# Kernel optimization log

Measured on AMD Instinct MI355X. Metric: run time of the kernel, lower is better.

The kernel has to match this reference:

```python
import jax, jax.numpy as jnp
import numpy as np

CHUNK = 2048  # query chunk for KNN to avoid materializing full NxN distance matrix


def _knn_single(pos, k):
    # pos: [N,3] -> idx [N,k] of k nearest neighbors (incl. self)
    N = pos.shape[0]
    qs = pos.reshape(N // CHUNK, CHUNK, 3)

    def per_chunk(q):
        d = jnp.sum((q[:, None, :] - pos[None, :, :]) ** 2, axis=-1)  # [CHUNK,N]
        _, idx = jax.lax.top_k(-d, k)
        return idx

    return jax.lax.map(per_chunk, qs).reshape(N, k)


def setup_inputs() -> dict:
    key = jax.random.key(0)
    ks = jax.random.split(key, 8)
    B, N, Cin, Cout, H, K = 2, 16384, 32, 64, 128, 16
    Ein = 2 * Cin + 3  # in_feat + out(self)_feat + rel_pos

    def lin(k_, fi, fo):
        return jax.random.normal(k_, (fi, fo), jnp.float32) / np.sqrt(fi)

    return dict(
        positions=jax.random.uniform(ks[0], (B, N, 3), jnp.float32),
        features=jax.random.normal(ks[1], (B, N, Cin), jnp.float32),
        W1=lin(ks[2], Ein, H), b1=jnp.zeros((H,), jnp.float32),
        W2=lin(ks[3], H, Cout), b2=jnp.zeros((Cout,), jnp.float32),
        W3=lin(ks[4], Cout, H), b3=jnp.zeros((H,), jnp.float32),
        W4=lin(ks[5], H, Cout), b4=jnp.zeros((Cout,), jnp.float32),
        knn_k=K,
    )


def reference(positions, features, W1, b1, W2, b2, W3, b3, W4, b4, knn_k):
    # 1) KNN neighbor search per batch
    idx = jax.vmap(lambda p: _knn_single(p, knn_k))(positions)  # [B,N,K]
    gather = jax.vmap(lambda a, i: a[i])
    # 2) gather neighbor features / positions
    nbr_feat = gather(features, idx)                      # [B,N,K,Cin]
    nbr_pos = gather(positions, idx)                      # [B,N,K,3]
    rel_pos = nbr_pos - positions[:, :, None, :]          # [B,N,K,3]
    self_feat = jnp.broadcast_to(features[:, :, None, :], nbr_feat.shape)
    # 3) edge features: cat(in_feat, out_feat, rel_pos)
    edge = jnp.concatenate([nbr_feat, self_feat, rel_pos], axis=-1)  # [B,N,K,Ein]
    # 4) edge MLP
    h = jax.nn.gelu(edge @ W1 + b1) @ W2 + b2             # [B,N,K,Cout]
    # 5) mean reduction over neighbors
    agg = jnp.mean(h, axis=2)                             # [B,N,Cout]
    # 6) output MLP
    return jax.nn.gelu(agg @ W3 + b3) @ W4 + b4           # [B,N,Cout]
```

## Files before the change

### kernel.cpp

```cpp
#include <hip/hip_runtime.h>
#include <math.h>

#define N_PTS 16384
#define BATCH 2
#define CIN   32
#define H_DIM 128
#define COUT  64
#define KNN   16
#define GC    16
#define NCELL (GC * GC * GC)
#define CS    (1.0f / GC)
#define PB    4
#define CHUNK 2048

typedef unsigned short ushortT;

__device__ __forceinline__ float gelu_f(float x) {
    float x3 = x * x * x;
    float t  = tanhf(0.7978845608028654f * (x + 0.044715f * x3));
    return 0.5f * x * (1.0f + t);
}
__device__ __forceinline__ float gelu_fast(float x) {
    float z = 1.5957691216057308f * (x + 0.044715f * x * x * x);
    return x / (1.0f + __expf(-z));
}

__device__ __forceinline__ int cellco(float v) {
    int c = (int)(v * (float)GC);
    return c < 0 ? 0 : (c > GC - 1 ? GC - 1 : c);
}

__global__ __launch_bounds__(256)
void zero_kernel(int* __restrict__ cnt) {
    cnt[blockIdx.x * 256 + threadIdx.x] = 0;
}

__global__ __launch_bounds__(256)
void count_kernel(const float* __restrict__ pos, int* __restrict__ cnt) {
    const int t = blockIdx.x * 256 + threadIdx.x;
    const int b = t >> 14;
    float x = pos[(size_t)t * 3 + 0];
    float y = pos[(size_t)t * 3 + 1];
    float z = pos[(size_t)t * 3 + 2];
    int cell = (cellco(z) * GC + cellco(y)) * GC + cellco(x);
    atomicAdd(&cnt[b * NCELL + cell], 1);
}

__global__ __launch_bounds__(1024)
void scan_kernel(const int* __restrict__ cnt, int* __restrict__ off,
                 int* __restrict__ cur) {
    __shared__ int s[1024];
    const int b = blockIdx.x;
    const int t = threadIdx.x;
    const int* c = cnt + b * NCELL;
    const int base = t * 4;
    int v0 = c[base], v1 = c[base + 1], v2 = c[base + 2], v3 = c[base + 3];
    int s01 = v0 + v1, s012 = s01 + v2, tot = s012 + v3;
    s[t] = tot;
    __syncthreads();
    for (int d = 1; d < 1024; d <<= 1) {
        int add = (t >= d) ? s[t - d] : 0;
        __syncthreads();
        s[t] += add;
        __syncthreads();
    }
    int excl = s[t] - tot;
    int* ob = off + b * (NCELL + 1);
    int* cb = cur + b * NCELL;
    ob[base] = excl;            cb[base] = excl;
    ob[base + 1] = excl + v0;   cb[base + 1] = excl + v0;
    ob[base + 2] = excl + s01;  cb[base + 2] = excl + s01;
    ob[base + 3] = excl + s012; cb[base + 3] = excl + s012;
    if (t == 1023) ob[NCELL] = excl + tot;
}

__global__ __launch_bounds__(256)
void scatter_kernel(const float* __restrict__ pos, int* __restrict__ cur,
                    float4* __restrict__ pos4) {
    const int t = blockIdx.x * 256 + threadIdx.x;
    const int b = t >> 14;
    const int pid = t & (N_PTS - 1);
    float x = pos[(size_t)t * 3 + 0];
    float y = pos[(size_t)t * 3 + 1];
    float z = pos[(size_t)t * 3 + 2];
    int cell = (cellco(z) * GC + cellco(y)) * GC + cellco(x);
    int slot = atomicAdd(&cur[b * NCELL + cell], 1);
    pos4[(size_t)b * N_PTS + slot] = make_float4(x, y, z, __int_as_float(pid));
}

__global__ __launch_bounds__(64)
void knnq_kernel(const float4* __restrict__ pos4,
                 const int* __restrict__ off, ushortT* __restrict__ out_idx) {
    __shared__ int soff[NCELL + 1];

    const int tid = threadIdx.x;
    const int t = blockIdx.x * 64 + tid;
    const int b = t >> 14;
    const int* offb = off + b * (NCELL + 1);
    for (int i = tid; i < NCELL + 1; i += 64) soff[i] = offb[i];

    const float4 Q = pos4[t];
    const float qx = Q.x, qy = Q.y, qz = Q.z;
    const int pid = __float_as_int(Q.w);
    const int cx = cellco(qx), cy = cellco(qy), cz = cellco(qz);
    const float4* p4b = pos4 + (size_t)b * N_PTS;
    __syncthreads();

    float ld[KNN]; int li[KNN];
#pragma unroll
    for (int p = 0; p < KNN; ++p) { ld[p] = 3.0e38f; li[p] = 0x7fffffff; }
    float t15d = 3.0e38f; int t15i = 0x7fffffff;

    auto scan_range = [&](int s, int e2) {
        for (int u = s; u < e2; u += 8) {
            float4 pg[8];
#pragma unroll
            for (int i = 0; i < 8; ++i) {
                int uu = u + i; uu = uu < e2 - 1 ? uu : e2 - 1;
                pg[i] = p4b[uu];
            }
#pragma unroll
            for (int i = 0; i < 8; ++i) {
                if (u + i >= e2) break;
                float ddx = __fsub_rn(qx, pg[i].x);
                float ddy = __fsub_rn(qy, pg[i].y);
                float ddz = __fsub_rn(qz, pg[i].z);
                float d = __fadd_rn(__fadd_rn(__fmul_rn(ddx, ddx),
                                              __fmul_rn(ddy, ddy)),
                                    __fmul_rn(ddz, ddz));
                int pj = __float_as_int(pg[i].w);
                if (d < t15d || (d == t15d && pj < t15i)) {
                    float cd = d; int cj = pj;
#pragma unroll
                    for (int p = 0; p < KNN; ++p) {
                        bool sw = (cd < ld[p]) || (cd == ld[p] && cj < li[p]);
                        float td = ld[p]; int ti = li[p];
                        ld[p] = sw ? cd : td; li[p] = sw ? cj : ti;
                        cd = sw ? td : cd;    cj = sw ? ti : cj;
                    }
                    t15d = ld[KNN - 1]; t15i = li[KNN - 1];
                }
            }
        }
    };

    for (int r = 1; r <= GC; ++r) {
        for (int dz = -r; dz <= r; ++dz) {
            const int Z = cz + dz; if ((unsigned)Z >= GC) continue;
            for (int dy = -r; dy <= r; ++dy) {
                const int Y = cy + dy; if ((unsigned)Y >= GC) continue;
                const int rowbase = (Z * GC + Y) * GC;
                const bool fullrow = (r == 1) ||
                    (dz == -r || dz == r || dy == -r || dy == r);
                if (fullrow) {
                    int X0 = cx - r; X0 = X0 < 0 ? 0 : X0;
                    int X1 = cx + r; X1 = X1 > GC - 1 ? GC - 1 : X1;
                    scan_range(soff[rowbase + X0], soff[rowbase + X1 + 1]);
                } else {
                    const int Xl = cx - r, Xr = cx + r;
                    if (Xl >= 0)
                        scan_range(soff[rowbase + Xl], soff[rowbase + Xl + 1]);
                    if (Xr <= GC - 1)
                        scan_range(soff[rowbase + Xr], soff[rowbase + Xr + 1]);
                }
            }
        }
        float mg = 1.0e19f;
        if (cx - r > 0)      mg = fminf(mg, qx - (float)(cx - r) * CS);
        if (cx + r < GC - 1) mg = fminf(mg, (float)(cx + r + 1) * CS - qx);
        if (cy - r > 0)      mg = fminf(mg, qy - (float)(cy - r) * CS);
        if (cy + r < GC - 1) mg = fminf(mg, (float)(cy + r + 1) * CS - qy);
        if (cz - r > 0)      mg = fminf(mg, qz - (float)(cz - r) * CS);
        if (cz + r < GC - 1) mg = fminf(mg, (float)(cz + r + 1) * CS - qz);
        if (t15d < mg * mg * 0.99999f) break;
    }
    ushortT* dst = out_idx + ((size_t)(b << 14) + pid) * KNN;
#pragma unroll
    for (int p = 0; p < KNN; ++p) dst[p] = (ushortT)li[p];
}

__global__ __launch_bounds__(256)
void feat1_kernel(const float* __restrict__ feats, const float* __restrict__ W1,
                  float* __restrict__ feat1) {
    const int g = blockIdx.x * 256 + threadIdx.x;
    const int p = g >> 7;
    const int h = g & 127;
    const float* fr = feats + (size_t)p * CIN;
    float a = 0.f;
#pragma unroll
    for (int c = 0; c < CIN; ++c)
        a += fr[c] * W1[c * H_DIM + h];
    feat1[g] = a;
}

__global__ __launch_bounds__(64)
void mlp2_kernel(const float* __restrict__ pos, const float* __restrict__ feats,
                 const ushortT* __restrict__ knn_idx, const float* __restrict__ feat1,
                 const float* __restrict__ W1, const float* __restrict__ b1,
                 const float* __restrict__ W2, const float* __restrict__ b2,
                 const float* __restrict__ W3, const float* __restrict__ b3,
                 const float* __restrict__ W4, const float* __restrict__ b4,
                 float* __restrict__ out) {
    __shared__ ushortT sIdx[PB][KNN];
    __shared__ float sq[PB][3];
    __shared__ __align__(16) float fself[PB][CIN];
    __shared__ float npx[PB][KNN][3];
    __shared__ __align__(16) float gs[PB][H_DIM];
    __shared__ __align__(16) float aggs[PB][COUT];
    __shared__ __align__(16) float hs[PB][H_DIM];

    const int tid = threadIdx.x;
    const int h0 = tid, h1 = tid + 64;
    const int i0 = blockIdx.x * PB;
    const size_t bofs = (size_t)(i0 >> 14) * N_PTS;

    for (int e = tid; e < PB * KNN; e += 64)
        sIdx[e >> 4][e & 15] = knn_idx[(size_t)(i0 + (e >> 4)) * KNN + (e & 15)];
    for (int e = tid; e < PB * 3; e += 64)
        sq[e / 3][e % 3] = pos[(size_t)(i0 + e / 3) * 3 + (e % 3)];
    for (int e = tid; e < PB * CIN; e += 64)
        fself[e >> 5][e & 31] = feats[(size_t)(i0 + (e >> 5)) * CIN + (e & 31)];
    __syncthreads();
    for (int e = tid; e < PB * KNN * 3; e += 64) {
        int p = e / (KNN * 3), r = e % (KNN * 3), k = r / 3, c = r % 3;
        npx[p][k][c] = pos[(bofs + sIdx[p][k]) * 3 + c];
    }

    const float w0A = W1[(2 * CIN + 0) * H_DIM + h0], w0B = W1[(2 * CIN + 0) * H_DIM + h1];
    const float w1A = W1[(2 * CIN + 1) * H_DIM + h0], w1B = W1[(2 * CIN + 1) * H_DIM + h1];
    const float w2A = W1[(2 * CIN + 2) * H_DIM + h0], w2B = W1[(2 * CIN + 2) * H_DIM + h1];
    float bA[PB], bB[PB];
#pragma unroll
    for (int p = 0; p < PB; ++p) { bA[p] = b1[h0]; bB[p] = b1[h1]; }
    __syncthreads();
#pragma unroll
    for (int c = 0; c < CIN; ++c) {
        float wA = W1[(CIN + c) * H_DIM + h0];
        float wB = W1[(CIN + c) * H_DIM + h1];
#pragma unroll
        for (int p = 0; p < PB; ++p) {
            bA[p] += fself[p][c] * wA;
            bB[p] += fself[p][c] * wB;
        }
    }

    float accA[PB] = {0.f, 0.f, 0.f, 0.f};
    float accB[PB] = {0.f, 0.f, 0.f, 0.f};
    for (int k = 0; k < KNN; ++k) {
#pragma unroll
        for (int p = 0; p < PB; ++p) {
            const float* fr = feat1 + (bofs + sIdx[p][k]) * H_DIM;
            float rx = npx[p][k][0] - sq[p][0];
            float ry = npx[p][k][1] - sq[p][1];
            float rz = npx[p][k][2] - sq[p][2];
            float uA = bA[p] + fr[h0] + rx * w0A + ry * w1A + rz * w2A;
            float uB = bB[p] + fr[h1] + rx * w0B + ry * w1B + rz * w2B;
            accA[p] += gelu_fast(uA);
            accB[p] += gelu_fast(uB);
        }
    }
#pragma unroll
    for (int p = 0; p < PB; ++p) {
        gs[p][h0] = accA[p] * (1.0f / KNN);
        gs[p][h1] = accB[p] * (1.0f / KNN);
    }
    __syncthreads();

    float a2[PB];
#pragma unroll
    for (int p = 0; p < PB; ++p) a2[p] = b2[h0];
    for (int c4 = 0; c4 < H_DIM / 4; ++c4) {
        float wx = W2[(4 * c4 + 0) * COUT + h0];
        float wy = W2[(4 * c4 + 1) * COUT + h0];
        float wz = W2[(4 * c4 + 2) * COUT + h0];
        float ww = W2[(4 * c4 + 3) * COUT + h0];
#pragma unroll
        for (int p = 0; p < PB; ++p) {
            float4 g = ((const float4*)gs[p])[c4];
            a2[p] += g.x * wx + g.y * wy + g.z * wz + g.w * ww;
        }
    }
#pragma unroll
    for (int p = 0; p < PB; ++p) aggs[p][h0] = a2[p];
    __syncthreads();

    float a3A[PB], a3B[PB];
#pragma unroll
    for (int p = 0; p < PB; ++p) { a3A[p] = b3[h0]; a3B[p] = b3[h1]; }
    for (int c4 = 0; c4 < COUT / 4; ++c4) {
        float wxA = W3[(4 * c4 + 0) * H_DIM + h0], wxB = W3[(4 * c4 + 0) * H_DIM + h1];
        float wyA = W3[(4 * c4 + 1) * H_DIM + h0], wyB = W3[(4 * c4 + 1) * H_DIM + h1];
        float wzA = W3[(4 * c4 + 2) * H_DIM + h0], wzB = W3[(4 * c4 + 2) * H_DIM + h1];
        float wwA = W3[(4 * c4 + 3) * H_DIM + h0], wwB = W3[(4 * c4 + 3) * H_DIM + h1];
#pragma unroll
        for (int p = 0; p < PB; ++p) {
            float4 g = ((const float4*)aggs[p])[c4];
            a3A[p] += g.x * wxA + g.y * wyA + g.z * wzA + g.w * wwA;
            a3B[p] += g.x * wxB + g.y * wyB + g.z * wzB + g.w * wwB;
        }
    }
#pragma unroll
    for (int p = 0; p < PB; ++p) {
        hs[p][h0] = gelu_fast(a3A[p]);
        hs[p][h1] = gelu_fast(a3B[p]);
    }
    __syncthreads();

    float o4[PB];
#pragma unroll
    for (int p = 0; p < PB; ++p) o4[p] = b4[h0];
    for (int c4 = 0; c4 < H_DIM / 4; ++c4) {
        float wx = W4[(4 * c4 + 0) * COUT + h0];
        float wy = W4[(4 * c4 + 1) * COUT + h0];
        float wz = W4[(4 * c4 + 2) * COUT + h0];
        float ww = W4[(4 * c4 + 3) * COUT + h0];
#pragma unroll
        for (int p = 0; p < PB; ++p) {
            float4 v = ((const float4*)hs[p])[c4];
            o4[p] += v.x * wx + v.y * wy + v.z * wz + v.w * ww;
        }
    }
#pragma unroll
    for (int p = 0; p < PB; ++p)
        out[(size_t)(i0 + p) * COUT + h0] = o4[p];
}

__global__ __launch_bounds__(64)
void mlp_kernel(const float* __restrict__ pos, const float* __restrict__ feats,
                const ushortT* __restrict__ knn_idx,
                const float* __restrict__ W1, const float* __restrict__ b1,
                const float* __restrict__ W2, const float* __restrict__ b2,
                const float* __restrict__ W3, const float* __restrict__ b3,
                const float* __restrict__ W4, const float* __restrict__ b4,
                float* __restrict__ out) {
    __shared__ ushortT sIdx[PB][KNN];
    __shared__ float sq[PB][3];
    __shared__ __align__(16) float fself[PB][CIN];
    __shared__ float npx[PB][KNN][3];
    __shared__ __align__(16) float nf[PB][KNN][CIN];
    __shared__ __align__(16) float gs[PB][H_DIM];
    __shared__ __align__(16) float aggs[PB][COUT];
    __shared__ __align__(16) float hs[PB][H_DIM];

    const int tid = threadIdx.x;
    const int h0 = tid, h1 = tid + 64;
    const int i0 = blockIdx.x * PB;
    const size_t bofs = (size_t)(i0 >> 14) * N_PTS;

    for (int e = tid; e < PB * KNN; e += 64)
        sIdx[e >> 4][e & 15] = knn_idx[(size_t)(i0 + (e >> 4)) * KNN + (e & 15)];
    for (int e = tid; e < PB * 3; e += 64)
        sq[e / 3][e % 3] = pos[(size_t)(i0 + e / 3) * 3 + (e % 3)];
    for (int e = tid; e < PB * CIN; e += 64)
        fself[e >> 5][e & 31] = feats[(size_t)(i0 + (e >> 5)) * CIN + (e & 31)];
    __syncthreads();
    for (int e = tid; e < PB * KNN * CIN; e += 64) {
        int p = e >> 9, k = (e >> 5) & 15, c = e & 31;
        nf[p][k][c] = feats[(bofs + sIdx[p][k]) * CIN + c];
    }
    for (int e = tid; e < PB * KNN * 3; e += 64) {
        int p = e / (KNN * 3), r = e % (KNN * 3), k = r / 3, c = r % 3;
        npx[p][k][c] = pos[(bofs + sIdx[p][k]) * 3 + c];
    }

    float w1rA[CIN], w1rB[CIN];
#pragma unroll
    for (int c = 0; c < CIN; ++c) {
        w1rA[c] = W1[c * H_DIM + h0];
        w1rB[c] = W1[c * H_DIM + h1];
    }
    const float w0A = W1[(2 * CIN + 0) * H_DIM + h0], w0B = W1[(2 * CIN + 0) * H_DIM + h1];
    const float w1A = W1[(2 * CIN + 1) * H_DIM + h0], w1B = W1[(2 * CIN + 1) * H_DIM + h1];
    const float w2A = W1[(2 * CIN + 2) * H_DIM + h0], w2B = W1[(2 * CIN + 2) * H_DIM + h1];
    float bA[PB], bB[PB];
#pragma unroll
    for (int p = 0; p < PB; ++p) { bA[p] = b1[h0]; bB[p] = b1[h1]; }
    __syncthreads();
#pragma unroll
    for (int c = 0; c < CIN; ++c) {
        float wA = W1[(CIN + c) * H_DIM + h0];
        float wB = W1[(CIN + c) * H_DIM + h1];
#pragma unroll
        for (int p = 0; p < PB; ++p) {
            bA[p] += fself[p][c] * wA;
            bB[p] += fself[p][c] * wB;
        }
    }

    float accA[PB] = {0.f, 0.f, 0.f, 0.f};
    float accB[PB] = {0.f, 0.f, 0.f, 0.f};
    for (int k = 0; k < KNN; ++k) {
#pragma unroll
        for (int p = 0; p < PB; ++p) {
            float rx = npx[p][k][0] - sq[p][0];
            float ry = npx[p][k][1] - sq[p][1];
            float rz = npx[p][k][2] - sq[p][2];
            float uA = bA[p] + rx * w0A + ry * w1A + rz * w2A;
            float uB = bB[p] + rx * w0B + ry * w1B + rz * w2B;
            const float4* nf4 = (const float4*)nf[p][k];
#pragma unroll
            for (int c4 = 0; c4 < CIN / 4; ++c4) {
                float4 v = nf4[c4];
                uA += v.x * w1rA[4 * c4] + v.y * w1rA[4 * c4 + 1]
                    + v.z * w1rA[4 * c4 + 2] + v.w * w1rA[4 * c4 + 3];
                uB += v.x * w1rB[4 * c4] + v.y * w1rB[4 * c4 + 1]
                    + v.z * w1rB[4 * c4 + 2] + v.w * w1rB[4 * c4 + 3];
            }
            accA[p] += gelu_f(uA);
            accB[p] += gelu_f(uB);
        }
    }
#pragma unroll
    for (int p = 0; p < PB; ++p) {
        gs[p][h0] = accA[p] * (1.0f / KNN);
        gs[p][h1] = accB[p] * (1.0f / KNN);
    }
    __syncthreads();

    float a2[PB];
#pragma unroll
    for (int p = 0; p < PB; ++p) a2[p] = b2[h0];
    for (int c4 = 0; c4 < H_DIM / 4; ++c4) {
        float wx = W2[(4 * c4 + 0) * COUT + h0];
        float wy = W2[(4 * c4 + 1) * COUT + h0];
        float wz = W2[(4 * c4 + 2) * COUT + h0];
        float ww = W2[(4 * c4 + 3) * COUT + h0];
#pragma unroll
        for (int p = 0; p < PB; ++p) {
            float4 g = ((const float4*)gs[p])[c4];
            a2[p] += g.x * wx + g.y * wy + g.z * wz + g.w * ww;
        }
    }
#pragma unroll
    for (int p = 0; p < PB; ++p) aggs[p][h0] = a2[p];
    __syncthreads();

    float a3A[PB], a3B[PB];
#pragma unroll
    for (int p = 0; p < PB; ++p) { a3A[p] = b3[h0]; a3B[p] = b3[h1]; }
    for (int c4 = 0; c4 < COUT / 4; ++c4) {
        float wxA = W3[(4 * c4 + 0) * H_DIM + h0], wxB = W3[(4 * c4 + 0) * H_DIM + h1];
        float wyA = W3[(4 * c4 + 1) * H_DIM + h0], wyB = W3[(4 * c4 + 1) * H_DIM + h1];
        float wzA = W3[(4 * c4 + 2) * H_DIM + h0], wzB = W3[(4 * c4 + 2) * H_DIM + h1];
        float wwA = W3[(4 * c4 + 3) * H_DIM + h0], wwB = W3[(4 * c4 + 3) * H_DIM + h1];
#pragma unroll
        for (int p = 0; p < PB; ++p) {
            float4 g = ((const float4*)aggs[p])[c4];
            a3A[p] += g.x * wxA + g.y * wyA + g.z * wzA + g.w * wwA;
            a3B[p] += g.x * wxB + g.y * wyB + g.z * wzB + g.w * wwB;
        }
    }
#pragma unroll
    for (int p = 0; p < PB; ++p) {
        hs[p][h0] = gelu_f(a3A[p]);
        hs[p][h1] = gelu_f(a3B[p]);
    }
    __syncthreads();

    float o4[PB];
#pragma unroll
    for (int p = 0; p < PB; ++p) o4[p] = b4[h0];
    for (int c4 = 0; c4 < H_DIM / 4; ++c4) {
        float wx = W4[(4 * c4 + 0) * COUT + h0];
        float wy = W4[(4 * c4 + 1) * COUT + h0];
        float wz = W4[(4 * c4 + 2) * COUT + h0];
        float ww = W4[(4 * c4 + 3) * COUT + h0];
#pragma unroll
        for (int p = 0; p < PB; ++p) {
            float4 v = ((const float4*)hs[p])[c4];
            o4[p] += v.x * wx + v.y * wy + v.z * wz + v.w * ww;
        }
    }
#pragma unroll
    for (int p = 0; p < PB; ++p)
        out[(size_t)(i0 + p) * COUT + h0] = o4[p];
}

#define NT    128
#define LP    17
__global__ __launch_bounds__(NT)
void fused_kernel(const float* __restrict__ pos, const float* __restrict__ feats,
                  const float* __restrict__ W1, const float* __restrict__ b1,
                  const float* __restrict__ W2, const float* __restrict__ b2,
                  const float* __restrict__ W3, const float* __restrict__ b3,
                  const float* __restrict__ W4, const float* __restrict__ b4,
                  float* __restrict__ out) {
    __shared__ float sx[CHUNK], sy[CHUNK], sz[CHUNK];
    __shared__ float ld0[NT * LP]; __shared__ int li0[NT * LP];
    __shared__ float ld1[NT * LP]; __shared__ int li1[NT * LP];
    __shared__ int   sIdx[KNN];
    __shared__ float npx[KNN][3];
    __shared__ float nf[KNN][CIN];
    __shared__ float fself[CIN];
    __shared__ float gs[H_DIM];
    __shared__ float aggs[COUT];
    __shared__ float hs[H_DIM];

    const int i   = blockIdx.x;
    const int b   = i >> 14;
    const int tid = threadIdx.x;
    const float* posb = pos + (size_t)b * N_PTS * 3;

    const float qx = pos[(size_t)i * 3 + 0];
    const float qy = pos[(size_t)i * 3 + 1];
    const float qz = pos[(size_t)i * 3 + 2];

    const int base = tid * LP;
    for (int s = 0; s < KNN; ++s) { ld0[base + s] = 3.0e38f; li0[base + s] = 0x7fffffff; }
    float taild = 3.0e38f;

    for (int cbase = 0; cbase < N_PTS; cbase += CHUNK) {
        __syncthreads();
        for (int t = tid; t < CHUNK * 3; t += NT) {
            float v = posb[(size_t)cbase * 3 + t];
            int c = t % 3, r = t / 3;
            (c == 0 ? sx : (c == 1 ? sy : sz))[r] = v;
        }
        __syncthreads();
        for (int r = tid; r < CHUNK; r += NT) {
            float dx = __fsub_rn(qx, sx[r]);
            float dy = __fsub_rn(qy, sy[r]);
            float dz = __fsub_rn(qz, sz[r]);
            float d  = __fadd_rn(__fadd_rn(__fmul_rn(dx, dx), __fmul_rn(dy, dy)),
                                 __fmul_rn(dz, dz));
            const int j = cbase + r;
            if (d < taild) {
                int p = KNN - 1;
                while (p > 0) {
                    float pd = ld0[base + p - 1];
                    if (!(pd > d)) break;
                    ld0[base + p] = pd;
                    li0[base + p] = li0[base + p - 1];
                    --p;
                }
                ld0[base + p] = d;
                li0[base + p] = j;
                taild = ld0[base + KNN - 1];
            }
        }
    }

    int cur = 0;
    for (int s = 1; s < NT; s <<= 1) {
        __syncthreads();
        if ((tid & (2 * s - 1)) == 0) {
            const float* cd  = cur ? ld1 : ld0;
            const int*   cix = cur ? li1 : li0;
            float* nd  = cur ? ld0 : ld1;
            int*   nix = cur ? li0 : li1;
            const int A = tid * LP, B = (tid + s) * LP, O = tid * LP;
            int a = 0, bb = 0;
            for (int o = 0; o < KNN; ++o) {
                float da = cd[A + a], db = cd[B + bb];
                int   ia = cix[A + a], ib = cix[B + bb];
                bool tA = (da < db) || (da == db && ia < ib);
                nd[O + o]  = tA ? da : db;
                nix[O + o] = tA ? ia : ib;
                a += tA ? 1 : 0; bb += tA ? 0 : 1;
            }
        }
        cur ^= 1;
    }
    __syncthreads();
    {
        const int* fli = cur ? li1 : li0;
        if (tid < KNN) sIdx[tid] = fli[tid];
        if (tid < CIN) fself[tid] = feats[(size_t)i * CIN + tid];
    }
    __syncthreads();

    for (int e = tid; e < KNN * CIN; e += NT) {
        int k = e >> 5, c = e & 31;
        nf[k][c] = feats[((size_t)b * N_PTS + sIdx[k]) * CIN + c];
    }
    if (tid < KNN * 3) {
        int k = tid / 3, c = tid % 3;
        npx[k][c] = posb[sIdx[k] * 3 + c];
    }
    const int h = tid;
    float w1r[CIN];
#pragma unroll
    for (int c = 0; c < CIN; ++c) w1r[c] = W1[c * H_DIM + h];
    float baseh = b1[h];
    const float w0 = W1[(2 * CIN + 0) * H_DIM + h];
    const float w1 = W1[(2 * CIN + 1) * H_DIM + h];
    const float w2 = W1[(2 * CIN + 2) * H_DIM + h];
#pragma unroll
    for (int c = 0; c < CIN; ++c)
        baseh += fself[c] * W1[(CIN + c) * H_DIM + h];
    __syncthreads();

    float acc = 0.f;
    for (int k = 0; k < KNN; ++k) {
        float u = baseh
                + (npx[k][0] - qx) * w0
                + (npx[k][1] - qy) * w1
                + (npx[k][2] - qz) * w2;
#pragma unroll
        for (int c = 0; c < CIN; ++c)
            u += nf[k][c] * w1r[c];
        acc += gelu_f(u);
    }
    gs[h] = acc * (1.0f / KNN);
    __syncthreads();

    if (h < COUT) {
        float a = b2[h];
#pragma unroll
        for (int t2 = 0; t2 < H_DIM; ++t2)
            a += gs[t2] * W2[t2 * COUT + h];
        aggs[h] = a;
    }
    __syncthreads();

    float a3 = b3[h];
#pragma unroll
    for (int c = 0; c < COUT; ++c)
        a3 += aggs[c] * W3[c * H_DIM + h];
    hs[h] = gelu_f(a3);
    __syncthreads();
    if (h < COUT) {
        float o = b4[h];
#pragma unroll
        for (int t2 = 0; t2 < H_DIM; ++t2)
            o += hs[t2] * W4[t2 * COUT + h];
        out[(size_t)i * COUT + h] = o;
    }
}

extern "C" void kernel_launch(void* const* d_in, const int* in_sizes, int n_in,
                              void* d_out, int out_size, void* d_ws, size_t ws_size,
                              hipStream_t stream) {
    const float* pos   = (const float*)d_in[0];
    const float* feats = (const float*)d_in[1];
    const float* W1    = (const float*)d_in[2];
    const float* b1    = (const float*)d_in[3];
    const float* W2    = (const float*)d_in[4];
    const float* b2    = (const float*)d_in[5];
    const float* W3    = (const float*)d_in[6];
    const float* b3    = (const float*)d_in[7];
    const float* W4    = (const float*)d_in[8];
    const float* b4    = (const float*)d_in[9];
    float* out = (float*)d_out;

    const int M = BATCH * N_PTS;

    char* ws = (char*)d_ws;
    const size_t need_small = (size_t)1536 * 1024 + 97 * 1024;
    const size_t need_big   = (size_t)18 * 1024 * 1024;

    if (ws_size >= need_small && d_ws != nullptr) {
        ushortT* idx  = (ushortT*)ws;
        float4*  pos4 = (float4*)(ws + (size_t)1024 * 1024);
        int*     cnt  = (int*)(ws + (size_t)1536 * 1024);
        int*     off  = (int*)(ws + (size_t)1536 * 1024 + 32 * 1024);
        int*     curp = (int*)(ws + (size_t)1536 * 1024 + 65 * 1024);

        zero_kernel   <<<(BATCH * NCELL) / 256, 256, 0, stream>>>(cnt);
        count_kernel  <<<M / 256, 256, 0, stream>>>(pos, cnt);
        scan_kernel   <<<BATCH, 1024, 0, stream>>>(cnt, off, curp);
        scatter_kernel<<<M / 256, 256, 0, stream>>>(pos, curp, pos4);
        knnq_kernel   <<<M / 64, 64, 0, stream>>>(pos4, off, idx);

        if (ws_size >= need_big) {
            float* feat1 = (float*)(ws + (size_t)2 * 1024 * 1024);
            feat1_kernel<<<(M * H_DIM) / 256, 256, 0, stream>>>(feats, W1, feat1);
            mlp2_kernel <<<M / PB, 64, 0, stream>>>(pos, feats, idx, feat1,
                                                    W1, b1, W2, b2, W3, b3, W4, b4, out);
        } else {
            mlp_kernel  <<<M / PB, 64, 0, stream>>>(pos, feats, idx,
                                                    W1, b1, W2, b2, W3, b3, W4, b4, out);
        }
    } else {
        fused_kernel<<<M, NT, 0, stream>>>(pos, feats, W1, b1, W2, b2,
                                           W3, b3, W4, b4, out);
    }
}
```

Baseline: 387.6 us.

## Process MLP points in spatially sorted cell order for gather locality

The scatter kernel now records each point's sorted slot, and the per-point projected features are stored in cell-sorted order. The MLP kernel walks points in sorted order and maps neighbor ids to slots, so the neighbor gathers of feat1 and positions hit nearby rows. This is meant to cut scattered global reads and improve cache hit rates. The cost is an extra indirection (knn_idx then slot_of), and output writes that become scattered by pid.

```diff
diff --git a/kernel.cpp b/kernel.cpp
--- a/kernel.cpp
+++ b/kernel.cpp
@@ -76,7 +76,7 @@
 
 __global__ __launch_bounds__(256)
 void scatter_kernel(const float* __restrict__ pos, int* __restrict__ cur,
-                    float4* __restrict__ pos4) {
+                    float4* __restrict__ pos4, ushortT* __restrict__ slot_of) {
     const int t = blockIdx.x * 256 + threadIdx.x;
     const int b = t >> 14;
     const int pid = t & (N_PTS - 1);
@@ -86,6 +86,7 @@
     int cell = (cellco(z) * GC + cellco(y)) * GC + cellco(x);
     int slot = atomicAdd(&cur[b * NCELL + cell], 1);
     pos4[(size_t)b * N_PTS + slot] = make_float4(x, y, z, __int_as_float(pid));
+    slot_of[(size_t)b * N_PTS + pid] = (ushortT)slot;
 }
 
 __global__ __launch_bounds__(64)
@@ -180,28 +181,32 @@
 }
 
 __global__ __launch_bounds__(256)
-void feat1_kernel(const float* __restrict__ feats, const float* __restrict__ W1,
-                  float* __restrict__ feat1) {
+void feat1s_kernel(const float4* __restrict__ pos4, const float* __restrict__ feats,
+                   const float* __restrict__ W1, float* __restrict__ feat1s) {
     const int g = blockIdx.x * 256 + threadIdx.x;
-    const int p = g >> 7;
+    const int s = g >> 7;
     const int h = g & 127;
-    const float* fr = feats + (size_t)p * CIN;
+    const int b = s >> 14;
+    const int pid = __float_as_int(pos4[s].w);
+    const float* fr = feats + ((size_t)b * N_PTS + pid) * CIN;
     float a = 0.f;
 #pragma unroll
     for (int c = 0; c < CIN; ++c)
         a += fr[c] * W1[c * H_DIM + h];
-    feat1[g] = a;
+    feat1s[(size_t)s * H_DIM + h] = a;
 }
 
 __global__ __launch_bounds__(64)
-void mlp2_kernel(const float* __restrict__ pos, const float* __restrict__ feats,
-                 const ushortT* __restrict__ knn_idx, const float* __restrict__ feat1,
-                 const float* __restrict__ W1, const float* __restrict__ b1,
-                 const float* __restrict__ W2, const float* __restrict__ b2,
-                 const float* __restrict__ W3, const float* __restrict__ b3,
-                 const float* __restrict__ W4, const float* __restrict__ b4,
-                 float* __restrict__ out) {
+void mlp2s_kernel(const float4* __restrict__ pos4, const float* __restrict__ feats,
+                  const ushortT* __restrict__ knn_idx, const ushortT* __restrict__ slot_of,
+                  const float* __restrict__ feat1s,
+                  const float* __restrict__ W1, const float* __restrict__ b1,
+                  const float* __restrict__ W2, const float* __restrict__ b2,
+                  const float* __restrict__ W3, const float* __restrict__ b3,
+                  const float* __restrict__ W4, const float* __restrict__ b4,
+                  float* __restrict__ out) {
     __shared__ ushortT sIdx[PB][KNN];
+    __shared__ int   spid[PB];
     __shared__ float sq[PB][3];
     __shared__ __align__(16) float fself[PB][CIN];
     __shared__ float npx[PB][KNN][3];
@@ -212,18 +217,27 @@
     const int tid = threadIdx.x;
     const int h0 = tid, h1 = tid + 64;
     const int i0 = blockIdx.x * PB;
-    const size_t bofs = (size_t)(i0 >> 14) * N_PTS;
-
-    for (int e = tid; e < PB * KNN; e += 64)
-        sIdx[e >> 4][e & 15] = knn_idx[(size_t)(i0 + (e >> 4)) * KNN + (e & 15)];
-    for (int e = tid; e < PB * 3; e += 64)
-        sq[e / 3][e % 3] = pos[(size_t)(i0 + e / 3) * 3 + (e % 3)];
+    const int b  = i0 >> 14;
+    const size_t bofs = (size_t)b * N_PTS;
+
+    if (tid < PB) {
+        float4 P = pos4[i0 + tid];
+        sq[tid][0] = P.x; sq[tid][1] = P.y; sq[tid][2] = P.z;
+        spid[tid] = __float_as_int(P.w);
+    }
+    __syncthreads();
+    for (int e = tid; e < PB * KNN; e += 64) {
+        int p = e >> 4, k = e & 15;
+        int npid = knn_idx[(bofs + spid[p]) * KNN + k];
+        sIdx[p][k] = slot_of[bofs + npid];
+    }
     for (int e = tid; e < PB * CIN; e += 64)
-        fself[e >> 5][e & 31] = feats[(size_t)(i0 + (e >> 5)) * CIN + (e & 31)];
-    __syncthreads();
-    for (int e = tid; e < PB * KNN * 3; e += 64) {
-        int p = e / (KNN * 3), r = e % (KNN * 3), k = r / 3, c = r % 3;
-        npx[p][k][c] = pos[(bofs + sIdx[p][k]) * 3 + c];
+        fself[e >> 5][e & 31] = feats[(bofs + spid[e >> 5]) * CIN + (e & 31)];
+    __syncthreads();
+    for (int e = tid; e < PB * KNN; e += 64) {
+        int p = e >> 4, k = e & 15;
+        float4 P = pos4[bofs + sIdx[p][k]];
+        npx[p][k][0] = P.x; npx[p][k][1] = P.y; npx[p][k][2] = P.z;
     }
 
     const float w0A = W1[(2 * CIN + 0) * H_DIM + h0], w0B = W1[(2 * CIN + 0) * H_DIM + h1];
@@ -249,7 +263,7 @@
     for (int k = 0; k < KNN; ++k) {
 #pragma unroll
         for (int p = 0; p < PB; ++p) {
-            const float* fr = feat1 + (bofs + sIdx[p][k]) * H_DIM;
+            const float* fr = feat1s + ((size_t)bofs + sIdx[p][k]) * H_DIM;
             float rx = npx[p][k][0] - sq[p][0];
             float ry = npx[p][k][1] - sq[p][1];
             float rz = npx[p][k][2] - sq[p][2];
@@ -322,7 +336,7 @@
     }
 #pragma unroll
     for (int p = 0; p < PB; ++p)
-        out[(size_t)(i0 + p) * COUT + h0] = o4[p];
+        out[((size_t)bofs + spid[p]) * COUT + h0] = o4[p];
 }
 
 __global__ __launch_bounds__(64)
@@ -646,30 +660,31 @@
     const int M = BATCH * N_PTS;
 
     char* ws = (char*)d_ws;
-    const size_t need_small = (size_t)1536 * 1024 + 97 * 1024;
+    const size_t need_small = (size_t)1536 * 1024 + 161 * 1024;
     const size_t need_big   = (size_t)18 * 1024 * 1024;
 
     if (ws_size >= need_small && d_ws != nullptr) {
-        ushortT* idx  = (ushortT*)ws;
-        float4*  pos4 = (float4*)(ws + (size_t)1024 * 1024);
-        int*     cnt  = (int*)(ws + (size_t)1536 * 1024);
-        int*     off  = (int*)(ws + (size_t)1536 * 1024 + 32 * 1024);
-        int*     curp = (int*)(ws + (size_t)1536 * 1024 + 65 * 1024);
+        ushortT* idx   = (ushortT*)ws;
+        float4*  pos4  = (float4*)(ws + (size_t)1024 * 1024);
+        int*     cnt   = (int*)(ws + (size_t)1536 * 1024);
+        int*     off   = (int*)(ws + (size_t)1536 * 1024 + 32 * 1024);
+        int*     curp  = (int*)(ws + (size_t)1536 * 1024 + 65 * 1024);
+        ushortT* slotf = (ushortT*)(ws + (size_t)1536 * 1024 + 97 * 1024);
 
         zero_kernel   <<<(BATCH * NCELL) / 256, 256, 0, stream>>>(cnt);
         count_kernel  <<<M / 256, 256, 0, stream>>>(pos, cnt);
         scan_kernel   <<<BATCH, 1024, 0, stream>>>(cnt, off, curp);
-        scatter_kernel<<<M / 256, 256, 0, stream>>>(pos, curp, pos4);
+        scatter_kernel<<<M / 256, 256, 0, stream>>>(pos, curp, pos4, slotf);
         knnq_kernel   <<<M / 64, 64, 0, stream>>>(pos4, off, idx);
 
         if (ws_size >= need_big) {
-            float* feat1 = (float*)(ws + (size_t)2 * 1024 * 1024);
-            feat1_kernel<<<(M * H_DIM) / 256, 256, 0, stream>>>(feats, W1, feat1);
-            mlp2_kernel <<<M / PB, 64, 0, stream>>>(pos, feats, idx, feat1,
-                                                    W1, b1, W2, b2, W3, b3, W4, b4, out);
+            float* feat1s = (float*)(ws + (size_t)2 * 1024 * 1024);
+            feat1s_kernel<<<(M * H_DIM) / 256, 256, 0, stream>>>(pos4, feats, W1, feat1s);
+            mlp2s_kernel <<<M / PB, 64, 0, stream>>>(pos4, feats, idx, slotf, feat1s,
+                                                     W1, b1, W2, b2, W3, b3, W4, b4, out);
         } else {
-            mlp_kernel  <<<M / PB, 64, 0, stream>>>(pos, feats, idx,
-                                                    W1, b1, W2, b2, W3, b3, W4, b4, out);
+            mlp_kernel   <<<M / PB, 64, 0, stream>>>(pos, feats, idx,
+                                                     W1, b1, W2, b2, W3, b3, W4, b4, out);
         }
     } else {
         fused_kernel<<<M, NT, 0, stream>>>(pos, feats, W1, b1, W2, b2,
```

New measurement: 384.8 us. About the same (-0.7%).
